# Optimization experiments

Hardware: AMD Instinct MI355X
Metric: run time of the kernel (lower is better)

Reference implementation:

```python
import jax, jax.numpy as jnp
import numpy as np

K, D, Q, N = 32, 256, 16, 8192


def setup_inputs() -> dict:
    key = jax.random.key(0)
    kx, km, kl = jax.random.split(key, 3)
    X = jax.random.normal(kx, (N, D), dtype=jnp.float32)
    # mirrors MFA.__init__ parameter init
    log_pi = jnp.full((K,), -jnp.log(jnp.float32(K)), dtype=jnp.float32)
    mu = 0.1 * jax.random.normal(km, (K, D), dtype=jnp.float32)
    Lambda = 0.1 * jax.random.normal(kl, (K, D, Q), dtype=jnp.float32)
    log_psi = jnp.full((D,), jnp.log(jnp.float32(0.01)), dtype=jnp.float32)
    return {"X": X, "log_pi": log_pi, "mu": mu, "Lambda": Lambda, "log_psi": log_psi}


def reference(X, log_pi, mu, Lambda, log_psi):
    """Batched-over-K translation of MFA.e_step (full-cov Cholesky log_prob)."""
    psi = jnp.exp(log_psi) + 1e-6                       # [D]
    eye = jnp.eye(D, dtype=X.dtype)
    # C_k = Lambda_k Lambda_k^T + diag(psi) + 1e-5 I    -> [K, D, D]
    C = jnp.einsum('kdq,keq->kde', Lambda, Lambda) + (jnp.diag(psi) + 1e-5 * eye)[None]
    L = jnp.linalg.cholesky(C)                          # [K, D, D]
    diff = X[None, :, :] - mu[:, None, :]               # [K, N, D]
    # whiten: solve L y = (x - mu)^T  -> [K, D, N]
    y = jax.scipy.linalg.solve_triangular(L, jnp.swapaxes(diff, 1, 2), lower=True)
    maha = jnp.sum(y * y, axis=1)                       # [K, N]
    logdet = 2.0 * jnp.sum(jnp.log(jnp.diagonal(L, axis1=1, axis2=2)), axis=1)  # [K]
    log2pi = jnp.log(jnp.asarray(2.0 * np.pi, dtype=X.dtype))
    log_prob = -0.5 * (D * log2pi + logdet[:, None] + maha)  # [K, N]
    log_resps = log_prob.T + log_pi[None, :]            # [N, K]
    log_likelihood = jax.nn.logsumexp(log_resps, axis=1)  # [N]
    log_resp_norm = log_resps - log_likelihood[:, None]
    return log_resp_norm, log_likelihood
```

## Files before the change

kernel.cpp:

```cpp
#include <hip/hip_runtime.h>
#include <math.h>

#define KK 32
#define DD 256
#define QQ 16
#define NN 8192
#define LOG2PI 1.8378770664093453f
#define NCT 36
#define GS_STRIDE 580

typedef __attribute__((ext_vector_type(8))) short short8v;
typedef __attribute__((ext_vector_type(4))) float float4v;

__device__ __forceinline__ unsigned short f2bf(float f) {
    union { float f; unsigned int u; } v; v.f = f;
    unsigned int u = v.u;
    return (unsigned short)((u + 0x7FFFu + ((u >> 16) & 1u)) >> 16);
}

__global__ __launch_bounds__(256) void mfa_setup_k(
    const float* __restrict__ log_pi,
    const float* __restrict__ mu,
    const float* __restrict__ Lambda,
    const float* __restrict__ log_psi,
    unsigned short* __restrict__ Wb,
    float* __restrict__ constk2,
    float* __restrict__ wvec)
{
    __shared__ float inv_a_s[DD];
    __shared__ float Ls[DD][QQ];
    __shared__ float Ms[QQ][QQ + 1];
    __shared__ float Lc[QQ][QQ + 1];
    __shared__ float Li[QQ][QQ + 1];
    __shared__ float red_lg[4], red_m2[4], redq[4][QQ];
    __shared__ float sum_log_a_s, mu2a_s;

    const int k = blockIdx.x;
    const int tid = threadIdx.x;
    const int wv = tid >> 6;

    const float a = expf(log_psi[tid]) + 1e-6f + 1e-5f;
    const float ia = 1.0f / a;
    inv_a_s[tid] = ia;
    const float mud = mu[k * DD + tid];

    float lg = logf(a);
    float m2 = mud * mud * ia;
    #pragma unroll
    for (int off = 32; off; off >>= 1) {
        lg += __shfl_down(lg, off, 64);
        m2 += __shfl_down(m2, off, 64);
    }
    if ((tid & 63) == 0) { red_lg[wv] = lg; red_m2[wv] = m2; }

    const float* Lk = Lambda + (size_t)k * DD * QQ;
    for (int i = tid; i < DD * QQ; i += 256) Ls[i >> 4][i & 15] = Lk[i];
    __syncthreads();
    if (tid == 0) {
        sum_log_a_s = red_lg[0] + red_lg[1] + red_lg[2] + red_lg[3];
        mu2a_s      = red_m2[0] + red_m2[1] + red_m2[2] + red_m2[3];
    }

    {
        const int q1 = tid >> 4, q2 = tid & 15;
        float b = 0.f;
        for (int d = 0; d < DD; ++d) b += Ls[d][q1] * Ls[d][q2] * inv_a_s[d];
        Ms[q1][q2] = b + (q1 == q2 ? 1.0f : 0.0f);
    }
    __syncthreads();

    for (int j = 0; j < QQ; ++j) {
        float s_i = 0.f;
        if (tid < QQ && tid >= j) {
            s_i = Ms[tid][j];
            for (int t = 0; t < j; ++t) s_i -= Lc[tid][t] * Lc[j][t];
        }
        if (tid == j) Lc[j][j] = sqrtf(s_i);
        __syncthreads();
        if (tid < QQ && tid > j) Lc[tid][j] = s_i / Lc[j][j];
        __syncthreads();
    }

    if (tid < QQ) {
        const int c = tid;
        for (int i = 0; i < c; ++i) Li[i][c] = 0.f;
        Li[c][c] = 1.0f / Lc[c][c];
        for (int i = c + 1; i < QQ; ++i) {
            float t = 0.f;
            for (int m = c; m < i; ++m) t -= Lc[i][m] * Li[m][c];
            Li[i][c] = t / Lc[i][i];
        }
    }
    __syncthreads();

    if (tid == 0) {
        float ld = 0.f;
        for (int j = 0; j < QQ; ++j) ld += logf(Lc[j][j]);
        const float logdetC = sum_log_a_s + 2.0f * ld;
        constk2[k] = log_pi[k] - 0.5f * ((float)DD * LOG2PI + logdetC + mu2a_s);
    }

    float tv[QQ];
    {
        float lam[QQ];
        #pragma unroll
        for (int q = 0; q < QQ; ++q) lam[q] = Ls[tid][q];
        #pragma unroll
        for (int q = 0; q < QQ; ++q) {
            float t = 0.f;
            for (int qp = 0; qp <= q; ++qp) t += Li[q][qp] * lam[qp];
            tv[q] = t * ia;
        }
    }

    #pragma unroll
    for (int q = 0; q < QQ; ++q) {
        float v = tv[q] * mud;
        #pragma unroll
        for (int off = 32; off; off >>= 1) v += __shfl_down(v, off, 64);
        if ((tid & 63) == 0) redq[wv][q] = v;
    }
    __syncthreads();
    if (tid < QQ) wvec[k * QQ + tid] = redq[0][tid] + redq[1][tid] + redq[2][tid] + redq[3][tid];

    {
        const int d = tid;
        const int kt = d >> 5, l_hi = (d >> 3) & 3, j = d & 7;
        #pragma unroll
        for (int q = 0; q < QQ; ++q) {
            const size_t idx = (((size_t)(kt * NCT + k) * 64) + l_hi * 16 + q) * 8 + j;
            Wb[idx] = f2bf(tv[q]);
        }
        const size_t idx = (((size_t)(kt * NCT + 32 + (k >> 4)) * 64) + l_hi * 16 + (k & 15)) * 8 + j;
        Wb[idx] = f2bf(mud * ia);
    }
    if (k < 2) {
        for (int i = tid; i < 512; i += 256) {
            const int kt = i >> 6, lane = i & 63;
            const size_t base = ((size_t)(kt * NCT + 34 + k) * 64 + lane) * 8;
            #pragma unroll
            for (int j = 0; j < 8; ++j) Wb[base + j] = 0;
        }
    }
}

__global__ __launch_bounds__(256) void mfa_gemm_fused(
    const float* __restrict__ X,
    const float* __restrict__ log_psi,
    const unsigned short* __restrict__ Wb,
    const float* __restrict__ constk2,
    const float* __restrict__ wvec,
    float* __restrict__ out)
{
    __shared__ float inv_a_s[DD];
    __shared__ float Gs[32][GS_STRIDE];
    __shared__ float w_s[KK][QQ];
    __shared__ float lps[32][KK + 1];
    __shared__ float sx_s[32];
    __shared__ float ck_s[KK];

    const int tid = threadIdx.x;
    const int lane = tid & 63, wv = tid >> 6;
    const int r0 = blockIdx.x * 32;

    inv_a_s[tid] = 1.0f / (expf(log_psi[tid]) + 1e-6f + 1e-5f);
    if (tid < KK) ck_s[tid] = constk2[tid];
    for (int i = tid; i < KK * QQ; i += 256) ((float*)w_s)[i] = wvec[i];
    __syncthreads();

    const int sw = wv * 9;
    float4v acc[2][9];
    #pragma unroll
    for (int rt = 0; rt < 2; ++rt)
        #pragma unroll
        for (int ct = 0; ct < 9; ++ct)
            #pragma unroll
            for (int r = 0; r < 4; ++r) acc[rt][ct][r] = 0.f;

    const int rA = r0 + (lane & 15);
    const int kq = (lane >> 4) * 8;
    const float* Xrow0 = X + (size_t)rA * DD;
    const float* Xrow1 = X + (size_t)(rA + 16) * DD;

    #pragma unroll
    for (int kt = 0; kt < 8; ++kt) {
        const int dbase = kt * 32 + kq;
        short8v bf[9];
        const short8v* Wp = (const short8v*)Wb + (size_t)(kt * NCT + sw) * 64 + lane;
        #pragma unroll
        for (int ct = 0; ct < 9; ++ct) bf[ct] = Wp[ct * 64];

        const float4 xa0 = *(const float4*)(Xrow0 + dbase);
        const float4 xa1 = *(const float4*)(Xrow0 + dbase + 4);
        const float4 xb0 = *(const float4*)(Xrow1 + dbase);
        const float4 xb1 = *(const float4*)(Xrow1 + dbase + 4);
        short8v a0, a1;
        a0[0] = (short)f2bf(xa0.x); a0[1] = (short)f2bf(xa0.y);
        a0[2] = (short)f2bf(xa0.z); a0[3] = (short)f2bf(xa0.w);
        a0[4] = (short)f2bf(xa1.x); a0[5] = (short)f2bf(xa1.y);
        a0[6] = (short)f2bf(xa1.z); a0[7] = (short)f2bf(xa1.w);
        a1[0] = (short)f2bf(xb0.x); a1[1] = (short)f2bf(xb0.y);
        a1[2] = (short)f2bf(xb0.z); a1[3] = (short)f2bf(xb0.w);
        a1[4] = (short)f2bf(xb1.x); a1[5] = (short)f2bf(xb1.y);
        a1[6] = (short)f2bf(xb1.z); a1[7] = (short)f2bf(xb1.w);

        #pragma unroll
        for (int ct = 0; ct < 9; ++ct) {
            acc[0][ct] = __builtin_amdgcn_mfma_f32_16x16x32_bf16(a0, bf[ct], acc[0][ct], 0, 0, 0);
            acc[1][ct] = __builtin_amdgcn_mfma_f32_16x16x32_bf16(a1, bf[ct], acc[1][ct], 0, 0, 0);
        }
    }

    {
        const int crow = (lane >> 4) * 4;
        const int ccol = lane & 15;
        #pragma unroll
        for (int rt = 0; rt < 2; ++rt)
            #pragma unroll
            for (int ct = 0; ct < 9; ++ct) {
                const int col = (sw + ct) * 16 + ccol;
                #pragma unroll
                for (int r = 0; r < 4; ++r)
                    Gs[rt * 16 + crow + r][col] = acc[rt][ct][r];
            }
    }

    {
        const int n = tid >> 3, part = tid & 7;
        const float4* xp = (const float4*)(X + (size_t)(r0 + n) * DD + part * 32);
        float s = 0.f;
        #pragma unroll
        for (int i = 0; i < 8; ++i) {
            const float4 v = xp[i];
            const int d = part * 32 + i * 4;
            s = fmaf(v.x * inv_a_s[d + 0], v.x, s);
            s = fmaf(v.y * inv_a_s[d + 1], v.y, s);
            s = fmaf(v.z * inv_a_s[d + 2], v.z, s);
            s = fmaf(v.w * inv_a_s[d + 3], v.w, s);
        }
        s += __shfl_xor(s, 1, 64);
        s += __shfl_xor(s, 2, 64);
        s += __shfl_xor(s, 4, 64);
        if (part == 0) sx_s[n] = s;
    }
    __syncthreads();

    #pragma unroll
    for (int it = 0; it < 4; ++it) {
        const int pp = it * 256 + tid;
        const int n = pp & 31, k = pp >> 5;
        const float4* zp = (const float4*)&Gs[n][k * QQ];
        float corr = 0.f;
        #pragma unroll
        for (int qq = 0; qq < 4; ++qq) {
            const float4 z = zp[qq];
            const float d0 = z.x - w_s[k][qq * 4 + 0];
            const float d1 = z.y - w_s[k][qq * 4 + 1];
            const float d2 = z.z - w_s[k][qq * 4 + 2];
            const float d3 = z.w - w_s[k][qq * 4 + 3];
            corr = fmaf(d0, d0, corr); corr = fmaf(d1, d1, corr);
            corr = fmaf(d2, d2, corr); corr = fmaf(d3, d3, corr);
        }
        const float xmu = Gs[n][512 + k];
        lps[n][k] = ck_s[k] - 0.5f * sx_s[n] + xmu + 0.5f * corr;
    }
    __syncthreads();

    if (tid < 32) {
        const int n = tid;
        float m = -INFINITY;
        #pragma unroll
        for (int k = 0; k < KK; ++k) m = fmaxf(m, lps[n][k]);
        float sum = 0.f;
        #pragma unroll
        for (int k = 0; k < KK; ++k) sum += expf(lps[n][k] - m);
        const float lse = m + logf(sum);
        float4* o = (float4*)(out + (size_t)(r0 + n) * KK);
        #pragma unroll
        for (int k4 = 0; k4 < KK / 4; ++k4)
            o[k4] = make_float4(lps[n][4 * k4 + 0] - lse, lps[n][4 * k4 + 1] - lse,
                                lps[n][4 * k4 + 2] - lse, lps[n][4 * k4 + 3] - lse);
        out[(size_t)NN * KK + r0 + n] = lse;
    }
}

extern "C" void kernel_launch(void* const* d_in, const int* in_sizes, int n_in,
                              void* d_out, int out_size, void* d_ws, size_t ws_size,
                              hipStream_t stream) {
    const float* X       = (const float*)d_in[0];
    const float* log_pi  = (const float*)d_in[1];
    const float* mu      = (const float*)d_in[2];
    const float* Lambda  = (const float*)d_in[3];
    const float* log_psi = (const float*)d_in[4];
    float* out = (float*)d_out;

    unsigned short* Wb = (unsigned short*)d_ws;
    float* constk2 = (float*)((char*)d_ws + 294912);
    float* wvec    = constk2 + KK;

    mfa_setup_k<<<KK, 256, 0, stream>>>(log_pi, mu, Lambda, log_psi, Wb, constk2, wvec);
    mfa_gemm_fused<<<NN / 32, 256, 0, stream>>>(X, log_psi, Wb, constk2, wvec, out);
}
```

Before: 101.3 us.

## Shrink GEMM tile to 16 rows, stage bf16 X in LDS, reduce in registers

The fused GEMM kernel now processes 16 rows per block instead of 32. It converts X to bf16 once into LDS, then computes the Mahalanobis correction directly from the MFMA accumulators using cross-lane shuffles. This drops the large fp32 G staging buffer in shared memory, which should cut LDS use and register pressure and raise occupancy, at the cost of twice as many blocks and reloading the W operand for each smaller tile. The setup kernel is also reworked: the 16x16 Cholesky factorisation becomes a shuffle-based register version with far fewer barriers, and the explicit inverse is replaced by forward substitution.

```diff
diff --git a/kernel.cpp b/kernel.cpp
--- a/kernel.cpp
+++ b/kernel.cpp
@@ -7,7 +7,7 @@
 #define NN 8192
 #define LOG2PI 1.8378770664093453f
 #define NCT 36
-#define GS_STRIDE 580
+#define CPW 9
 
 typedef __attribute__((ext_vector_type(8))) short short8v;
 typedef __attribute__((ext_vector_type(4))) float float4v;
@@ -29,11 +29,11 @@
 {
     __shared__ float inv_a_s[DD];
     __shared__ float Ls[DD][QQ];
+    __shared__ float Lsia[DD][QQ];
     __shared__ float Ms[QQ][QQ + 1];
     __shared__ float Lc[QQ][QQ + 1];
-    __shared__ float Li[QQ][QQ + 1];
     __shared__ float red_lg[4], red_m2[4], redq[4][QQ];
-    __shared__ float sum_log_a_s, mu2a_s;
+    __shared__ float sum_log_a_s, mu2a_s, ld_s;
 
     const int k = blockIdx.x;
     const int tid = threadIdx.x;
@@ -56,61 +56,70 @@
     const float* Lk = Lambda + (size_t)k * DD * QQ;
     for (int i = tid; i < DD * QQ; i += 256) Ls[i >> 4][i & 15] = Lk[i];
     __syncthreads();
+
+    #pragma unroll
+    for (int q = 0; q < QQ; ++q) Lsia[tid][q] = Ls[tid][q] * ia;
     if (tid == 0) {
         sum_log_a_s = red_lg[0] + red_lg[1] + red_lg[2] + red_lg[3];
         mu2a_s      = red_m2[0] + red_m2[1] + red_m2[2] + red_m2[3];
     }
+    __syncthreads();
 
     {
         const int q1 = tid >> 4, q2 = tid & 15;
         float b = 0.f;
-        for (int d = 0; d < DD; ++d) b += Ls[d][q1] * Ls[d][q2] * inv_a_s[d];
+        for (int d = 0; d < DD; ++d) b = fmaf(Lsia[d][q1], Ls[d][q2], b);
         Ms[q1][q2] = b + (q1 == q2 ? 1.0f : 0.0f);
     }
     __syncthreads();
 
-    for (int j = 0; j < QQ; ++j) {
-        float s_i = 0.f;
-        if (tid < QQ && tid >= j) {
-            s_i = Ms[tid][j];
-            for (int t = 0; t < j; ++t) s_i -= Lc[tid][t] * Lc[j][t];
-        }
-        if (tid == j) Lc[j][j] = sqrtf(s_i);
-        __syncthreads();
-        if (tid < QQ && tid > j) Lc[tid][j] = s_i / Lc[j][j];
-        __syncthreads();
-    }
-
     if (tid < QQ) {
-        const int c = tid;
-        for (int i = 0; i < c; ++i) Li[i][c] = 0.f;
-        Li[c][c] = 1.0f / Lc[c][c];
-        for (int i = c + 1; i < QQ; ++i) {
-            float t = 0.f;
-            for (int m = c; m < i; ++m) t -= Lc[i][m] * Li[m][c];
-            Li[i][c] = t / Lc[i][i];
-        }
+        const int i = tid;
+        float mrow[QQ];
+        #pragma unroll
+        for (int j = 0; j < QQ; ++j) mrow[j] = Ms[i][j];
+        float l[QQ];
+        float ldiag = 0.f;
+        #pragma unroll
+        for (int j = 0; j < QQ; ++j) {
+            float s = mrow[j];
+            #pragma unroll
+            for (int t = 0; t < QQ; ++t) {
+                if (t < j) s = fmaf(-l[t], __shfl(l[t], j, 64), s);
+            }
+            const float piv = __shfl(s, j, 64);
+            const float ljj = sqrtf(piv);
+            const float val = s / ljj;
+            l[j] = (i == j) ? ljj : ((i > j) ? val : 0.f);
+            if (i == j) ldiag = logf(ljj);
+        }
+        #pragma unroll
+        for (int j = 0; j < QQ; ++j) Lc[i][j] = l[j];
+        #pragma unroll
+        for (int mask = 1; mask <= 8; mask <<= 1) ldiag += __shfl_xor(ldiag, mask, 64);
+        if (i == 0) ld_s = ldiag;
     }
     __syncthreads();
 
     if (tid == 0) {
-        float ld = 0.f;
-        for (int j = 0; j < QQ; ++j) ld += logf(Lc[j][j]);
-        const float logdetC = sum_log_a_s + 2.0f * ld;
+        const float logdetC = sum_log_a_s + 2.0f * ld_s;
         constk2[k] = log_pi[k] - 0.5f * ((float)DD * LOG2PI + logdetC + mu2a_s);
     }
 
     float tv[QQ];
     {
-        float lam[QQ];
-        #pragma unroll
-        for (int q = 0; q < QQ; ++q) lam[q] = Ls[tid][q];
+        float y[QQ];
         #pragma unroll
         for (int q = 0; q < QQ; ++q) {
-            float t = 0.f;
-            for (int qp = 0; qp <= q; ++qp) t += Li[q][qp] * lam[qp];
-            tv[q] = t * ia;
-        }
+            float s = Ls[tid][q];
+            #pragma unroll
+            for (int m = 0; m < QQ; ++m) {
+                if (m < q) s = fmaf(-Lc[q][m], y[m], s);
+            }
+            y[q] = s / Lc[q][q];
+        }
+        #pragma unroll
+        for (int q = 0; q < QQ; ++q) tv[q] = y[q] * ia;
     }
 
     #pragma unroll
@@ -152,87 +161,64 @@
     const float* __restrict__ wvec,
     float* __restrict__ out)
 {
+    __shared__ short As[8 * 64 * 8];
     __shared__ float inv_a_s[DD];
-    __shared__ float Gs[32][GS_STRIDE];
     __shared__ float w_s[KK][QQ];
-    __shared__ float lps[32][KK + 1];
-    __shared__ float sx_s[32];
     __shared__ float ck_s[KK];
+    __shared__ float sx_s[16];
+    __shared__ float corr_s[16][KK + 1];
+    __shared__ float xmu_s[16][KK + 1];
 
     const int tid = threadIdx.x;
     const int lane = tid & 63, wv = tid >> 6;
-    const int r0 = blockIdx.x * 32;
+    const int r0 = blockIdx.x * 16;
 
     inv_a_s[tid] = 1.0f / (expf(log_psi[tid]) + 1e-6f + 1e-5f);
     if (tid < KK) ck_s[tid] = constk2[tid];
     for (int i = tid; i < KK * QQ; i += 256) ((float*)w_s)[i] = wvec[i];
-    __syncthreads();
-
-    const int sw = wv * 9;
-    float4v acc[2][9];
-    #pragma unroll
-    for (int rt = 0; rt < 2; ++rt)
-        #pragma unroll
-        for (int ct = 0; ct < 9; ++ct)
-            #pragma unroll
-            for (int r = 0; r < 4; ++r) acc[rt][ct][r] = 0.f;
-
-    const int rA = r0 + (lane & 15);
-    const int kq = (lane >> 4) * 8;
-    const float* Xrow0 = X + (size_t)rA * DD;
-    const float* Xrow1 = X + (size_t)(rA + 16) * DD;
+
+    #pragma unroll
+    for (int rep = 0; rep < 2; ++rep) {
+        const int c = tid + rep * 256;
+        const int kt = c >> 6, lc = c & 63;
+        const int m = lc & 15, d0 = kt * 32 + ((lc >> 4) & 3) * 8;
+        const float4* xp = (const float4*)(X + (size_t)(r0 + m) * DD + d0);
+        const float4 x0 = xp[0], x1 = xp[1];
+        short8v av;
+        av[0] = (short)f2bf(x0.x); av[1] = (short)f2bf(x0.y);
+        av[2] = (short)f2bf(x0.z); av[3] = (short)f2bf(x0.w);
+        av[4] = (short)f2bf(x1.x); av[5] = (short)f2bf(x1.y);
+        av[6] = (short)f2bf(x1.z); av[7] = (short)f2bf(x1.w);
+        *(short8v*)&As[(size_t)(kt * 64 + lc) * 8] = av;
+    }
+    __syncthreads();
+
+    const int sw = wv * CPW;
+    float4v acc[CPW];
+    #pragma unroll
+    for (int ct = 0; ct < CPW; ++ct)
+        #pragma unroll
+        for (int r = 0; r < 4; ++r) acc[ct][r] = 0.f;
 
     #pragma unroll
     for (int kt = 0; kt < 8; ++kt) {
-        const int dbase = kt * 32 + kq;
-        short8v bf[9];
+        const short8v a = *(const short8v*)&As[(size_t)(kt * 64 + lane) * 8];
         const short8v* Wp = (const short8v*)Wb + (size_t)(kt * NCT + sw) * 64 + lane;
         #pragma unroll
-        for (int ct = 0; ct < 9; ++ct) bf[ct] = Wp[ct * 64];
-
-        const float4 xa0 = *(const float4*)(Xrow0 + dbase);
-        const float4 xa1 = *(const float4*)(Xrow0 + dbase + 4);
-        const float4 xb0 = *(const float4*)(Xrow1 + dbase);
-        const float4 xb1 = *(const float4*)(Xrow1 + dbase + 4);
-        short8v a0, a1;
-        a0[0] = (short)f2bf(xa0.x); a0[1] = (short)f2bf(xa0.y);
-        a0[2] = (short)f2bf(xa0.z); a0[3] = (short)f2bf(xa0.w);
-        a0[4] = (short)f2bf(xa1.x); a0[5] = (short)f2bf(xa1.y);
-        a0[6] = (short)f2bf(xa1.z); a0[7] = (short)f2bf(xa1.w);
-        a1[0] = (short)f2bf(xb0.x); a1[1] = (short)f2bf(xb0.y);
-        a1[2] = (short)f2bf(xb0.z); a1[3] = (short)f2bf(xb0.w);
-        a1[4] = (short)f2bf(xb1.x); a1[5] = (short)f2bf(xb1.y);
-        a1[6] = (short)f2bf(xb1.z); a1[7] = (short)f2bf(xb1.w);
-
-        #pragma unroll
-        for (int ct = 0; ct < 9; ++ct) {
-            acc[0][ct] = __builtin_amdgcn_mfma_f32_16x16x32_bf16(a0, bf[ct], acc[0][ct], 0, 0, 0);
-            acc[1][ct] = __builtin_amdgcn_mfma_f32_16x16x32_bf16(a1, bf[ct], acc[1][ct], 0, 0, 0);
+        for (int ct = 0; ct < CPW; ++ct) {
+            const short8v bf = Wp[ct * 64];
+            acc[ct] = __builtin_amdgcn_mfma_f32_16x16x32_bf16(a, bf, acc[ct], 0, 0, 0);
         }
     }
 
     {
-        const int crow = (lane >> 4) * 4;
-        const int ccol = lane & 15;
-        #pragma unroll
-        for (int rt = 0; rt < 2; ++rt)
-            #pragma unroll
-            for (int ct = 0; ct < 9; ++ct) {
-                const int col = (sw + ct) * 16 + ccol;
-                #pragma unroll
-                for (int r = 0; r < 4; ++r)
-                    Gs[rt * 16 + crow + r][col] = acc[rt][ct][r];
-            }
-    }
-
-    {
-        const int n = tid >> 3, part = tid & 7;
-        const float4* xp = (const float4*)(X + (size_t)(r0 + n) * DD + part * 32);
+        const int n = tid >> 4, part = tid & 15;
+        const float4* xp = (const float4*)(X + (size_t)(r0 + n) * DD + part * 16);
         float s = 0.f;
         #pragma unroll
-        for (int i = 0; i < 8; ++i) {
+        for (int i = 0; i < 4; ++i) {
             const float4 v = xp[i];
-            const int d = part * 32 + i * 4;
+            const int d = part * 16 + i * 4;
             s = fmaf(v.x * inv_a_s[d + 0], v.x, s);
             s = fmaf(v.y * inv_a_s[d + 1], v.y, s);
             s = fmaf(v.z * inv_a_s[d + 2], v.z, s);
@@ -241,45 +227,59 @@
         s += __shfl_xor(s, 1, 64);
         s += __shfl_xor(s, 2, 64);
         s += __shfl_xor(s, 4, 64);
+        s += __shfl_xor(s, 8, 64);
         if (part == 0) sx_s[n] = s;
     }
-    __syncthreads();
-
-    #pragma unroll
-    for (int it = 0; it < 4; ++it) {
-        const int pp = it * 256 + tid;
-        const int n = pp & 31, k = pp >> 5;
-        const float4* zp = (const float4*)&Gs[n][k * QQ];
-        float corr = 0.f;
-        #pragma unroll
-        for (int qq = 0; qq < 4; ++qq) {
-            const float4 z = zp[qq];
-            const float d0 = z.x - w_s[k][qq * 4 + 0];
-            const float d1 = z.y - w_s[k][qq * 4 + 1];
-            const float d2 = z.z - w_s[k][qq * 4 + 2];
-            const float d3 = z.w - w_s[k][qq * 4 + 3];
-            corr = fmaf(d0, d0, corr); corr = fmaf(d1, d1, corr);
-            corr = fmaf(d2, d2, corr); corr = fmaf(d3, d3, corr);
-        }
-        const float xmu = Gs[n][512 + k];
-        lps[n][k] = ck_s[k] - 0.5f * sx_s[n] + xmu + 0.5f * corr;
-    }
-    __syncthreads();
-
-    if (tid < 32) {
+
+    #pragma unroll
+    for (int ct = 0; ct < CPW; ++ct) {
+        const int cti = sw + ct;
+        if (cti < 32) {
+            const float w = w_s[cti][lane & 15];
+            float q0 = acc[ct][0] - w, q1 = acc[ct][1] - w,
+                  q2 = acc[ct][2] - w, q3 = acc[ct][3] - w;
+            q0 *= q0; q1 *= q1; q2 *= q2; q3 *= q3;
+            #pragma unroll
+            for (int mask = 1; mask <= 8; mask <<= 1) {
+                q0 += __shfl_xor(q0, mask, 64);
+                q1 += __shfl_xor(q1, mask, 64);
+                q2 += __shfl_xor(q2, mask, 64);
+                q3 += __shfl_xor(q3, mask, 64);
+            }
+            if ((lane & 15) == 0) {
+                const int nb = (lane >> 4) * 4;
+                corr_s[nb + 0][cti] = q0; corr_s[nb + 1][cti] = q1;
+                corr_s[nb + 2][cti] = q2; corr_s[nb + 3][cti] = q3;
+            }
+        } else if (cti < 34) {
+            const int kk = (cti - 32) * 16 + (lane & 15);
+            const int nb = (lane >> 4) * 4;
+            xmu_s[nb + 0][kk] = acc[ct][0]; xmu_s[nb + 1][kk] = acc[ct][1];
+            xmu_s[nb + 2][kk] = acc[ct][2]; xmu_s[nb + 3][kk] = acc[ct][3];
+        }
+    }
+    __syncthreads();
+
+    if (tid < 16) {
         const int n = tid;
+        const float sxh = 0.5f * sx_s[n];
+        float lp[KK];
         float m = -INFINITY;
         #pragma unroll
-        for (int k = 0; k < KK; ++k) m = fmaxf(m, lps[n][k]);
+        for (int k = 0; k < KK; ++k) {
+            const float v = ck_s[k] - sxh + xmu_s[n][k] + 0.5f * corr_s[n][k];
+            lp[k] = v;
+            m = fmaxf(m, v);
+        }
         float sum = 0.f;
         #pragma unroll
-        for (int k = 0; k < KK; ++k) sum += expf(lps[n][k] - m);
+        for (int k = 0; k < KK; ++k) sum += expf(lp[k] - m);
         const float lse = m + logf(sum);
         float4* o = (float4*)(out + (size_t)(r0 + n) * KK);
         #pragma unroll
         for (int k4 = 0; k4 < KK / 4; ++k4)
-            o[k4] = make_float4(lps[n][4 * k4 + 0] - lse, lps[n][4 * k4 + 1] - lse,
-                                lps[n][4 * k4 + 2] - lse, lps[n][4 * k4 + 3] - lse);
+            o[k4] = make_float4(lp[4 * k4 + 0] - lse, lp[4 * k4 + 1] - lse,
+                                lp[4 * k4 + 2] - lse, lp[4 * k4 + 3] - lse);
         out[(size_t)NN * KK + r0 + n] = lse;
     }
 }
@@ -299,5 +299,5 @@
     float* wvec    = constk2 + KK;
 
     mfa_setup_k<<<KK, 256, 0, stream>>>(log_pi, mu, Lambda, log_psi, Wb, constk2, wvec);
-    mfa_gemm_fused<<<NN / 32, 256, 0, stream>>>(X, log_psi, Wb, constk2, wvec, out);
+    mfa_gemm_fused<<<NN / 16, 256, 0, stream>>>(X, log_psi, Wb, constk2, wvec, out);
 }
```

Measured after the change: 93.04 us. 1.09x faster.
